# Performance work log

Measured on AMD Instinct MI355X. Metric: run time of the kernel, lower is better.

## Reference

```python
import jax, jax.numpy as jnp
import numpy as np

V, BLOCK, D, H, L = 32000, 2048, 768, 12, 4
B, T = 2, 2048
HD = D // H
FF = 4 * D


def setup_inputs() -> dict:
    key = jax.random.key(0)
    ks = jax.random.split(key, 20)
    s = 0.02
    inp = {
        "idx": jax.random.randint(ks[0], (B, T), 0, V),
        "tok_emb": jax.random.normal(ks[1], (V, D), jnp.float32) * s,
        "pos_emb": jax.random.normal(ks[2], (BLOCK, D), jnp.float32) * s,
        # per-layer stacked params (leading dim L); linear weights stored [in, out]
        "ln1_w": jnp.ones((L, D), jnp.float32),
        "ln1_b": jnp.zeros((L, D), jnp.float32),
        "Wqkv": jax.random.normal(ks[3], (L, D, 3 * D), jnp.float32) * s,
        "bqkv": jnp.zeros((L, 3 * D), jnp.float32),
        "Wproj": jax.random.normal(ks[4], (L, D, D), jnp.float32) * s,
        "bproj": jnp.zeros((L, D), jnp.float32),
        "ln2_w": jnp.ones((L, D), jnp.float32),
        "ln2_b": jnp.zeros((L, D), jnp.float32),
        "Wfc": jax.random.normal(ks[5], (L, D, FF), jnp.float32) * s,
        "bfc": jnp.zeros((L, FF), jnp.float32),
        "Wfc2": jax.random.normal(ks[6], (L, FF, D), jnp.float32) * s,
        "bfc2": jnp.zeros((L, D), jnp.float32),
        "lnf_w": jnp.ones((D,), jnp.float32),
        "lnf_b": jnp.zeros((D,), jnp.float32),
    }
    return inp


def _layernorm(x, w, b, eps=1e-5):
    mu = jnp.mean(x, axis=-1, keepdims=True)
    var = jnp.var(x, axis=-1, keepdims=True)
    return (x - mu) * jax.lax.rsqrt(var + eps) * w + b


def _attn(x, Wqkv, bqkv, Wproj, bproj):
    b, t, c = x.shape
    qkv = x @ Wqkv + bqkv  # [B,T,3D]
    q, k, v = jnp.split(qkv, 3, axis=-1)
    q = q.reshape(b, t, H, HD)
    k = k.reshape(b, t, H, HD)
    v = v.reshape(b, t, H, HD)
    scale = 1.0 / np.sqrt(HD)
    att = jnp.einsum("bthd,bshd->bhts", q, k) * scale  # [B,H,T,T]
    causal = jnp.tril(jnp.ones((t, t), bool))
    att = jnp.where(causal[None, None], att, -jnp.inf)
    att = jax.nn.softmax(att, axis=-1)
    out = jnp.einsum("bhts,bshd->bthd", att, v).reshape(b, t, c)
    return out @ Wproj + bproj


def reference(idx, tok_emb, pos_emb, ln1_w, ln1_b, Wqkv, bqkv, Wproj, bproj,
              ln2_w, ln2_b, Wfc, bfc, Wfc2, bfc2, lnf_w, lnf_b):
    t = idx.shape[1]
    x = tok_emb[idx] + pos_emb[:t][None]  # [B,T,D]
    for l in range(L):
        h = _layernorm(x, ln1_w[l], ln1_b[l])
        x = x + _attn(h, Wqkv[l], bqkv[l], Wproj[l], bproj[l])
        h = _layernorm(x, ln2_w[l], ln2_b[l])
        h = jax.nn.gelu(h @ Wfc[l] + bfc[l], approximate=False) @ Wfc2[l] + bfc2[l]
        x = x + h
    x = _layernorm(x, lnf_w, lnf_b)
    return x @ tok_emb.T  # tied head, [B,T,V]
```

## Files before the change

kernel.cpp:

```cpp
#include <hip/hip_runtime.h>
#include <math.h>

#define VOCAB  32000
#define DMODEL 768
#define NHEAD  12
#define NLAYER 4
#define BATCH  2
#define SEQ    2048
#define HEADD  64
#define FFDIM  3072
#define MROWS  (BATCH*SEQ)

typedef __attribute__((ext_vector_type(8))) short bf16x8;
typedef __attribute__((ext_vector_type(4))) float f32x4;

__device__ __forceinline__ unsigned short f2bf(float f) {
    union { float f; unsigned u; } v; v.f = f;
    unsigned r = v.u + 0x7fffu + ((v.u >> 16) & 1u);
    return (unsigned short)(r >> 16);
}

__device__ __forceinline__ bf16x8 pack8(const float* v) {
    union { unsigned short u[8]; bf16x8 v8; } un;
#pragma unroll
    for (int j = 0; j < 8; j++) un.u[j] = f2bf(v[j]);
    return un.v8;
}

__global__ void cvt_bf16_x4(const float* __restrict__ in, unsigned short* __restrict__ out, int n4) {
    int i = blockIdx.x * blockDim.x + threadIdx.x;
    if (i >= n4) return;
    float4 v = ((const float4*)in)[i];
    uint2 o;
    o.x = (unsigned)f2bf(v.x) | ((unsigned)f2bf(v.y) << 16);
    o.y = (unsigned)f2bf(v.z) | ((unsigned)f2bf(v.w) << 16);
    ((uint2*)out)[i] = o;
}

__global__ void transpose_cvt(const float* __restrict__ W, unsigned short* __restrict__ Wt,
                              int Kdim, int Ndim) {
    __shared__ float tile[32][33];
    int l  = blockIdx.z;
    int k0 = blockIdx.x * 32;
    int n0 = blockIdx.y * 32;
    const float* Wl = W + (size_t)l * Kdim * Ndim;
    unsigned short* Wtl = Wt + (size_t)l * Kdim * Ndim;
    int c = threadIdx.x & 31, r = threadIdx.x >> 5;
#pragma unroll
    for (int i = 0; i < 4; i++)
        tile[r + i * 8][c] = Wl[(size_t)(k0 + r + i * 8) * Ndim + n0 + c];
    __syncthreads();
#pragma unroll
    for (int i = 0; i < 4; i++)
        Wtl[(size_t)(n0 + r + i * 8) * Kdim + k0 + c] = f2bf(tile[c][r + i * 8]);
}

__global__ void embed_kernel(const int* __restrict__ idx, const float* __restrict__ tok,
                             const float* __restrict__ pos, float* __restrict__ x) {
    int row = blockIdx.x;
    int t = row & (SEQ - 1);
    int tr = idx[row];
    const float4* ts = (const float4*)(tok + (size_t)tr * DMODEL);
    const float4* ps = (const float4*)(pos + (size_t)t * DMODEL);
    float4* xs = (float4*)(x + (size_t)row * DMODEL);
    int i = threadIdx.x;
    float4 a = ts[i], b = ps[i];
    xs[i] = make_float4(a.x + b.x, a.y + b.y, a.z + b.z, a.w + b.w);
}

__global__ void layernorm_kernel(const float* __restrict__ x, const float* __restrict__ w,
                                 const float* __restrict__ b, unsigned short* __restrict__ out) {
    int row = blockIdx.x;
    const float* xr = x + (size_t)row * DMODEL;
    int t = threadIdx.x;
    float v0 = xr[t], v1 = xr[t + 256], v2 = xr[t + 512];
    float s = v0 + v1 + v2;
    float ss = v0 * v0 + v1 * v1 + v2 * v2;
#pragma unroll
    for (int off = 32; off >= 1; off >>= 1) {
        s  += __shfl_xor(s, off);
        ss += __shfl_xor(ss, off);
    }
    __shared__ float red[8];
    int wave = t >> 6, lane = t & 63;
    if (lane == 0) { red[wave] = s; red[wave + 4] = ss; }
    __syncthreads();
    s  = red[0] + red[1] + red[2] + red[3];
    ss = red[4] + red[5] + red[6] + red[7];
    float mu = s * (1.0f / DMODEL);
    float var = ss * (1.0f / DMODEL) - mu * mu;
    float rs = rsqrtf(var + 1e-5f);
    unsigned short* orow = out + (size_t)row * DMODEL;
    orow[t]       = f2bf((v0 - mu) * rs * w[t]       + b[t]);
    orow[t + 256] = f2bf((v1 - mu) * rs * w[t + 256] + b[t + 256]);
    orow[t + 512] = f2bf((v2 - mu) * rs * w[t + 512] + b[t + 512]);
}

template <bool GELU_, bool RESID_, bool OUTBF16_, bool BIAS_>
__global__ __launch_bounds__(256) void gemm_kernel(
    const unsigned short* __restrict__ A,
    const unsigned short* __restrict__ Bw,
    const float* __restrict__ bias,
    const float* resid,
    float* Cf, unsigned short* Cb,
    int Ndim, int Kdim) {
    const int bm = blockIdx.x * 128;
    const int bn = blockIdx.y * 128;
    __shared__ unsigned short As[128][40];
    __shared__ unsigned short Bs[128][40];
    int tid = threadIdx.x;
    int wave = tid >> 6, lane = tid & 63;
    int wm = (wave >> 1) * 64, wn = (wave & 1) * 64;
    int quad = lane >> 4, ln = lane & 15;
    f32x4 acc[4][4] = {};

    for (int k0 = 0; k0 < Kdim; k0 += 32) {
        __syncthreads();
#pragma unroll
        for (int i = 0; i < 2; i++) {
            int c = tid + i * 256;
            int r = c >> 2, col = (c & 3) * 8;
            bf16x8 av = *(const bf16x8*)(A  + (size_t)(bm + r) * Kdim + k0 + col);
            *(bf16x8*)(&As[r][col]) = av;
            bf16x8 bv = *(const bf16x8*)(Bw + (size_t)(bn + r) * Kdim + k0 + col);
            *(bf16x8*)(&Bs[r][col]) = bv;
        }
        __syncthreads();
        bf16x8 af[4], bfr[4];
#pragma unroll
        for (int tm = 0; tm < 4; tm++) af[tm]  = *(const bf16x8*)(&As[wm + tm * 16 + ln][quad * 8]);
#pragma unroll
        for (int tn = 0; tn < 4; tn++) bfr[tn] = *(const bf16x8*)(&Bs[wn + tn * 16 + ln][quad * 8]);
#pragma unroll
        for (int tm = 0; tm < 4; tm++)
#pragma unroll
            for (int tn = 0; tn < 4; tn++)
                acc[tm][tn] = __builtin_amdgcn_mfma_f32_16x16x32_bf16(af[tm], bfr[tn], acc[tm][tn], 0, 0, 0);
    }

#pragma unroll
    for (int tm = 0; tm < 4; tm++)
#pragma unroll
        for (int tn = 0; tn < 4; tn++)
#pragma unroll
            for (int r = 0; r < 4; r++) {
                int row = bm + wm + tm * 16 + quad * 4 + r;
                int col = bn + wn + tn * 16 + ln;
                float c = acc[tm][tn][r];
                if (BIAS_) c += bias[col];
                if (GELU_) c = 0.5f * c * (1.0f + erff(c * 0.70710678118654752f));
                if (RESID_) c += resid[(size_t)row * Ndim + col];
                if (OUTBF16_) Cb[(size_t)row * Ndim + col] = f2bf(c);
                else          Cf[(size_t)row * Ndim + col] = c;
            }
}

__global__ __launch_bounds__(256) void attn_kernel(const float* __restrict__ qkv,
                                                   unsigned short* __restrict__ out) {
    int qtile = blockIdx.x;
    int bh = blockIdx.y;
    int b = bh / NHEAD, h = bh % NHEAD;
    int q0 = qtile * 128;
    const float* base = qkv + (size_t)b * SEQ * (3 * DMODEL);

    __shared__ unsigned short Qs[128][72];
    __shared__ unsigned short Ks[64][72];
    __shared__ unsigned short Vs[64][72];
    __shared__ unsigned short Ps[128][72];

    int tid = threadIdx.x, wave = tid >> 6, lane = tid & 63;
    int quad = lane >> 4, ln = lane & 15;

    for (int c = tid; c < 1024; c += 256) {
        int r = c >> 3, col = (c & 7) * 8;
        const float* src = base + (size_t)(q0 + r) * (3 * DMODEL) + h * HEADD + col;
        float4 a = *(const float4*)src, bb = *(const float4*)(src + 4);
        float tmp[8] = {a.x, a.y, a.z, a.w, bb.x, bb.y, bb.z, bb.w};
        *(bf16x8*)(&Qs[r][col]) = pack8(tmp);
    }
    __syncthreads();

    bf16x8 qf[2][2];
#pragma unroll
    for (int tm = 0; tm < 2; tm++)
#pragma unroll
        for (int ks = 0; ks < 2; ks++)
            qf[tm][ks] = *(const bf16x8*)(&Qs[wave * 32 + tm * 16 + ln][ks * 32 + quad * 8]);

    f32x4 o[2][4] = {};
    float mst[8], lst[8];
#pragma unroll
    for (int i = 0; i < 8; i++) { mst[i] = -3.0e38f; lst[i] = 0.0f; }

    const float scale = 0.125f;
    int nkt = qtile * 2 + 2;

    for (int kt = 0; kt < nkt; kt++) {
        __syncthreads();
        for (int c = tid; c < 512; c += 256) {
            int r = c >> 3, col = (c & 7) * 8;
            const float* sk = base + (size_t)(kt * 64 + r) * (3 * DMODEL) + DMODEL + h * HEADD + col;
            float4 a = *(const float4*)sk, bb = *(const float4*)(sk + 4);
            float tmp[8] = {a.x, a.y, a.z, a.w, bb.x, bb.y, bb.z, bb.w};
            *(bf16x8*)(&Ks[r][col]) = pack8(tmp);
            const float* sv = base + (size_t)(kt * 64 + r) * (3 * DMODEL) + 2 * DMODEL + h * HEADD + col;
            float4 va = *(const float4*)sv, vb = *(const float4*)(sv + 4);
            float tv[8] = {va.x, va.y, va.z, va.w, vb.x, vb.y, vb.z, vb.w};
#pragma unroll
            for (int j = 0; j < 8; j++) Vs[col + j][r] = f2bf(tv[j]);
        }
        __syncthreads();

        f32x4 s[2][4];
#pragma unroll
        for (int tm = 0; tm < 2; tm++)
#pragma unroll
            for (int tn = 0; tn < 4; tn++) s[tm][tn] = (f32x4){0.f, 0.f, 0.f, 0.f};
        bf16x8 kf[4][2];
#pragma unroll
        for (int tn = 0; tn < 4; tn++)
#pragma unroll
            for (int ks = 0; ks < 2; ks++)
                kf[tn][ks] = *(const bf16x8*)(&Ks[tn * 16 + ln][ks * 32 + quad * 8]);
#pragma unroll
        for (int tm = 0; tm < 2; tm++)
#pragma unroll
            for (int tn = 0; tn < 4; tn++)
#pragma unroll
                for (int ks = 0; ks < 2; ks++)
                    s[tm][tn] = __builtin_amdgcn_mfma_f32_16x16x32_bf16(qf[tm][ks], kf[tn][ks], s[tm][tn], 0, 0, 0);

#pragma unroll
        for (int tm = 0; tm < 2; tm++)
#pragma unroll
            for (int tn = 0; tn < 4; tn++)
#pragma unroll
                for (int r = 0; r < 4; r++) {
                    int qi = q0 + wave * 32 + tm * 16 + quad * 4 + r;
                    int kj = kt * 64 + tn * 16 + ln;
                    float sv = s[tm][tn][r] * scale;
                    s[tm][tn][r] = (kj > qi) ? -3.0e38f : sv;
                }

#pragma unroll
        for (int tm = 0; tm < 2; tm++)
#pragma unroll
            for (int r = 0; r < 4; r++) {
                float mx = fmaxf(fmaxf(s[tm][0][r], s[tm][1][r]), fmaxf(s[tm][2][r], s[tm][3][r]));
#pragma unroll
                for (int msk = 1; msk <= 8; msk <<= 1) mx = fmaxf(mx, __shfl_xor(mx, msk));
                int ri = tm * 4 + r;
                float mnew = fmaxf(mst[ri], mx);
                float alpha = __expf(mst[ri] - mnew);
                mst[ri] = mnew;
                float psum = 0.f;
#pragma unroll
                for (int tn = 0; tn < 4; tn++) {
                    float p = __expf(s[tm][tn][r] - mnew);
                    s[tm][tn][r] = p;
                    psum += p;
                }
#pragma unroll
                for (int msk = 1; msk <= 8; msk <<= 1) psum += __shfl_xor(psum, msk);
                lst[ri] = lst[ri] * alpha + psum;
#pragma unroll
                for (int nd = 0; nd < 4; nd++) o[tm][nd][r] *= alpha;
            }

#pragma unroll
        for (int tm = 0; tm < 2; tm++)
#pragma unroll
            for (int tn = 0; tn < 4; tn++)
#pragma unroll
                for (int r = 0; r < 4; r++)
                    Ps[wave * 32 + tm * 16 + quad * 4 + r][tn * 16 + ln] = f2bf(s[tm][tn][r]);

        bf16x8 pf[2][2], vf[4][2];
#pragma unroll
        for (int tm = 0; tm < 2; tm++)
#pragma unroll
            for (int ks = 0; ks < 2; ks++)
                pf[tm][ks] = *(const bf16x8*)(&Ps[wave * 32 + tm * 16 + ln][ks * 32 + quad * 8]);
#pragma unroll
        for (int nd = 0; nd < 4; nd++)
#pragma unroll
            for (int ks = 0; ks < 2; ks++)
                vf[nd][ks] = *(const bf16x8*)(&Vs[nd * 16 + ln][ks * 32 + quad * 8]);
#pragma unroll
        for (int tm = 0; tm < 2; tm++)
#pragma unroll
            for (int nd = 0; nd < 4; nd++)
#pragma unroll
                for (int ks = 0; ks < 2; ks++)
                    o[tm][nd] = __builtin_amdgcn_mfma_f32_16x16x32_bf16(pf[tm][ks], vf[nd][ks], o[tm][nd], 0, 0, 0);
    }

#pragma unroll
    for (int tm = 0; tm < 2; tm++)
#pragma unroll
        for (int r = 0; r < 4; r++) {
            float inv = 1.0f / lst[tm * 4 + r];
            int trow = q0 + wave * 32 + tm * 16 + quad * 4 + r;
#pragma unroll
            for (int nd = 0; nd < 4; nd++) {
                int col = h * HEADD + nd * 16 + ln;
                out[(size_t)(b * SEQ + trow) * DMODEL + col] = f2bf(o[tm][nd][r] * inv);
            }
        }
}

extern "C" void kernel_launch(void* const* d_in, const int* in_sizes, int n_in,
                              void* d_out, int out_size, void* d_ws, size_t ws_size,
                              hipStream_t stream) {
    const int*   idx   = (const int*)  d_in[0];
    const float* tok   = (const float*)d_in[1];
    const float* pos   = (const float*)d_in[2];
    const float* ln1w  = (const float*)d_in[3];
    const float* ln1b  = (const float*)d_in[4];
    const float* Wqkv  = (const float*)d_in[5];
    const float* bqkv  = (const float*)d_in[6];
    const float* Wproj = (const float*)d_in[7];
    const float* bproj = (const float*)d_in[8];
    const float* ln2w  = (const float*)d_in[9];
    const float* ln2b  = (const float*)d_in[10];
    const float* Wfc   = (const float*)d_in[11];
    const float* bfc   = (const float*)d_in[12];
    const float* Wfc2  = (const float*)d_in[13];
    const float* bfc2  = (const float*)d_in[14];
    const float* lnfw  = (const float*)d_in[15];
    const float* lnfb  = (const float*)d_in[16];

    char* ob = (char*)d_out;
    float*          qkv    = (float*)(ob + 0);
    float*          x      = (float*)(ob + 37748736);
    unsigned short* ffact  = (unsigned short*)(ob + 50331648);
    unsigned short* attnb  = (unsigned short*)(ob + 75497472);
    unsigned short* WqkvT  = (unsigned short*)(ob + 81788928);
    unsigned short* WprojT = (unsigned short*)(ob + 95944704);
    unsigned short* WfcT   = (unsigned short*)(ob + 100663296);
    unsigned short* Wfc2T  = (unsigned short*)(ob + 119537664);
    unsigned short* tokT   = (unsigned short*)d_ws;
    unsigned short* lnout  = (unsigned short*)((char*)d_ws + 49152000);

    cvt_bf16_x4<<<24000, 256, 0, stream>>>(tok, tokT, VOCAB * DMODEL / 4);
    transpose_cvt<<<dim3(24, 72, NLAYER), 256, 0, stream>>>(Wqkv,  WqkvT,  DMODEL, 3 * DMODEL);
    transpose_cvt<<<dim3(24, 24, NLAYER), 256, 0, stream>>>(Wproj, WprojT, DMODEL, DMODEL);
    transpose_cvt<<<dim3(24, 96, NLAYER), 256, 0, stream>>>(Wfc,   WfcT,   DMODEL, FFDIM);
    transpose_cvt<<<dim3(96, 24, NLAYER), 256, 0, stream>>>(Wfc2,  Wfc2T,  FFDIM,  DMODEL);

    embed_kernel<<<MROWS, 192, 0, stream>>>(idx, tok, pos, x);

    for (int l = 0; l < NLAYER; l++) {
        layernorm_kernel<<<MROWS, 256, 0, stream>>>(x, ln1w + l * DMODEL, ln1b + l * DMODEL, lnout);
        gemm_kernel<false, false, false, true><<<dim3(32, 18), 256, 0, stream>>>(
            lnout, WqkvT + (size_t)l * 3 * DMODEL * DMODEL, bqkv + l * 3 * DMODEL,
            nullptr, qkv, nullptr, 3 * DMODEL, DMODEL);
        attn_kernel<<<dim3(16, BATCH * NHEAD), 256, 0, stream>>>(qkv, attnb);
        gemm_kernel<false, true, false, true><<<dim3(32, 6), 256, 0, stream>>>(
            attnb, WprojT + (size_t)l * DMODEL * DMODEL, bproj + l * DMODEL,
            x, x, nullptr, DMODEL, DMODEL);
        layernorm_kernel<<<MROWS, 256, 0, stream>>>(x, ln2w + l * DMODEL, ln2b + l * DMODEL, lnout);
        gemm_kernel<true, false, true, true><<<dim3(32, 24), 256, 0, stream>>>(
            lnout, WfcT + (size_t)l * FFDIM * DMODEL, bfc + l * FFDIM,
            nullptr, nullptr, ffact, FFDIM, DMODEL);
        gemm_kernel<false, true, false, true><<<dim3(32, 6), 256, 0, stream>>>(
            ffact, Wfc2T + (size_t)l * FFDIM * DMODEL, bfc2 + l * DMODEL,
            x, x, nullptr, DMODEL, FFDIM);
    }

    layernorm_kernel<<<MROWS, 256, 0, stream>>>(x, lnfw, lnfb, lnout);
    gemm_kernel<false, false, false, false><<<dim3(32, 250), 256, 0, stream>>>(
        lnout, tokT, nullptr, nullptr, (float*)d_out, nullptr, VOCAB, DMODEL);
}
```

Before: 2.332 ms.

## Use async global-to-LDS loads in GEMM and store QKV as bf16

The GEMM tile loads now use global_load_lds to copy 16-byte chunks straight into unpadded LDS tiles, skipping the round trip through registers. The QKV projection now writes bf16 instead of fp32, so the attention kernel reads half the bytes and no longer converts per tile. The output buffer offsets are repacked to match. Removing the LDS padding may cause bank conflicts on fragment reads, and bf16 QKV adds rounding before attention, though attention already converted to bf16.

```diff
diff --git a/kernel.cpp b/kernel.cpp
--- a/kernel.cpp
+++ b/kernel.cpp
@@ -20,11 +20,10 @@
     return (unsigned short)(r >> 16);
 }
 
-__device__ __forceinline__ bf16x8 pack8(const float* v) {
-    union { unsigned short u[8]; bf16x8 v8; } un;
-#pragma unroll
-    for (int j = 0; j < 8; j++) un.u[j] = f2bf(v[j]);
-    return un.v8;
+__device__ __forceinline__ void async_lds16(const unsigned short* g, unsigned short* l) {
+    __builtin_amdgcn_global_load_lds(
+        (const __attribute__((address_space(1))) unsigned int*)(const void*)g,
+        (__attribute__((address_space(3))) unsigned int*)(void*)l, 16, 0, 0);
 }
 
 __global__ void cvt_bf16_x4(const float* __restrict__ in, unsigned short* __restrict__ out, int n4) {
@@ -106,24 +105,23 @@
     int Ndim, int Kdim) {
     const int bm = blockIdx.x * 128;
     const int bn = blockIdx.y * 128;
-    __shared__ unsigned short As[128][40];
-    __shared__ unsigned short Bs[128][40];
+    __shared__ unsigned short As[128][32];
+    __shared__ unsigned short Bs[128][32];
     int tid = threadIdx.x;
     int wave = tid >> 6, lane = tid & 63;
     int wm = (wave >> 1) * 64, wn = (wave & 1) * 64;
     int quad = lane >> 4, ln = lane & 15;
+    int srow = lane >> 2;
+    int scol = (lane & 3) * 8;
     f32x4 acc[4][4] = {};
 
     for (int k0 = 0; k0 < Kdim; k0 += 32) {
         __syncthreads();
 #pragma unroll
         for (int i = 0; i < 2; i++) {
-            int c = tid + i * 256;
-            int r = c >> 2, col = (c & 3) * 8;
-            bf16x8 av = *(const bf16x8*)(A  + (size_t)(bm + r) * Kdim + k0 + col);
-            *(bf16x8*)(&As[r][col]) = av;
-            bf16x8 bv = *(const bf16x8*)(Bw + (size_t)(bn + r) * Kdim + k0 + col);
-            *(bf16x8*)(&Bs[r][col]) = bv;
+            int ch = (wave << 1) | i;
+            async_lds16(A  + (size_t)(bm + ch * 16 + srow) * Kdim + k0 + scol, &As[ch * 16][0]);
+            async_lds16(Bw + (size_t)(bn + ch * 16 + srow) * Kdim + k0 + scol, &Bs[ch * 16][0]);
         }
         __syncthreads();
         bf16x8 af[4], bfr[4];
@@ -155,13 +153,13 @@
             }
 }
 
-__global__ __launch_bounds__(256) void attn_kernel(const float* __restrict__ qkv,
+__global__ __launch_bounds__(256) void attn_kernel(const unsigned short* __restrict__ qkv,
                                                    unsigned short* __restrict__ out) {
     int qtile = blockIdx.x;
     int bh = blockIdx.y;
     int b = bh / NHEAD, h = bh % NHEAD;
     int q0 = qtile * 128;
-    const float* base = qkv + (size_t)b * SEQ * (3 * DMODEL);
+    const unsigned short* base = qkv + (size_t)b * SEQ * (3 * DMODEL);
 
     __shared__ unsigned short Qs[128][72];
     __shared__ unsigned short Ks[64][72];
@@ -173,10 +171,8 @@
 
     for (int c = tid; c < 1024; c += 256) {
         int r = c >> 3, col = (c & 7) * 8;
-        const float* src = base + (size_t)(q0 + r) * (3 * DMODEL) + h * HEADD + col;
-        float4 a = *(const float4*)src, bb = *(const float4*)(src + 4);
-        float tmp[8] = {a.x, a.y, a.z, a.w, bb.x, bb.y, bb.z, bb.w};
-        *(bf16x8*)(&Qs[r][col]) = pack8(tmp);
+        *(bf16x8*)(&Qs[r][col]) =
+            *(const bf16x8*)(base + (size_t)(q0 + r) * (3 * DMODEL) + h * HEADD + col);
     }
     __syncthreads();
 
@@ -199,15 +195,12 @@
         __syncthreads();
         for (int c = tid; c < 512; c += 256) {
             int r = c >> 3, col = (c & 7) * 8;
-            const float* sk = base + (size_t)(kt * 64 + r) * (3 * DMODEL) + DMODEL + h * HEADD + col;
-            float4 a = *(const float4*)sk, bb = *(const float4*)(sk + 4);
-            float tmp[8] = {a.x, a.y, a.z, a.w, bb.x, bb.y, bb.z, bb.w};
-            *(bf16x8*)(&Ks[r][col]) = pack8(tmp);
-            const float* sv = base + (size_t)(kt * 64 + r) * (3 * DMODEL) + 2 * DMODEL + h * HEADD + col;
-            float4 va = *(const float4*)sv, vb = *(const float4*)(sv + 4);
-            float tv[8] = {va.x, va.y, va.z, va.w, vb.x, vb.y, vb.z, vb.w};
-#pragma unroll
-            for (int j = 0; j < 8; j++) Vs[col + j][r] = f2bf(tv[j]);
+            *(bf16x8*)(&Ks[r][col]) =
+                *(const bf16x8*)(base + (size_t)(kt * 64 + r) * (3 * DMODEL) + DMODEL + h * HEADD + col);
+            union { bf16x8 v; unsigned short u[8]; } vv;
+            vv.v = *(const bf16x8*)(base + (size_t)(kt * 64 + r) * (3 * DMODEL) + 2 * DMODEL + h * HEADD + col);
+#pragma unroll
+            for (int j = 0; j < 8; j++) Vs[col + j][r] = vv.u[j];
         }
         __syncthreads();
 
@@ -331,14 +324,14 @@
     const float* lnfb  = (const float*)d_in[16];
 
     char* ob = (char*)d_out;
-    float*          qkv    = (float*)(ob + 0);
-    float*          x      = (float*)(ob + 37748736);
-    unsigned short* ffact  = (unsigned short*)(ob + 50331648);
-    unsigned short* attnb  = (unsigned short*)(ob + 75497472);
-    unsigned short* WqkvT  = (unsigned short*)(ob + 81788928);
-    unsigned short* WprojT = (unsigned short*)(ob + 95944704);
-    unsigned short* WfcT   = (unsigned short*)(ob + 100663296);
-    unsigned short* Wfc2T  = (unsigned short*)(ob + 119537664);
+    unsigned short* qkvb   = (unsigned short*)(ob + 0);
+    float*          x      = (float*)(ob + 18874368);
+    unsigned short* ffact  = (unsigned short*)(ob + 31457280);
+    unsigned short* attnb  = (unsigned short*)(ob + 56623104);
+    unsigned short* WqkvT  = (unsigned short*)(ob + 62914560);
+    unsigned short* WprojT = (unsigned short*)(ob + 77070336);
+    unsigned short* WfcT   = (unsigned short*)(ob + 81788928);
+    unsigned short* Wfc2T  = (unsigned short*)(ob + 100663296);
     unsigned short* tokT   = (unsigned short*)d_ws;
     unsigned short* lnout  = (unsigned short*)((char*)d_ws + 49152000);
 
@@ -352,10 +345,10 @@
 
     for (int l = 0; l < NLAYER; l++) {
         layernorm_kernel<<<MROWS, 256, 0, stream>>>(x, ln1w + l * DMODEL, ln1b + l * DMODEL, lnout);
-        gemm_kernel<false, false, false, true><<<dim3(32, 18), 256, 0, stream>>>(
+        gemm_kernel<false, false, true, true><<<dim3(32, 18), 256, 0, stream>>>(
             lnout, WqkvT + (size_t)l * 3 * DMODEL * DMODEL, bqkv + l * 3 * DMODEL,
-            nullptr, qkv, nullptr, 3 * DMODEL, DMODEL);
-        attn_kernel<<<dim3(16, BATCH * NHEAD), 256, 0, stream>>>(qkv, attnb);
+            nullptr, nullptr, qkvb, 3 * DMODEL, DMODEL);
+        attn_kernel<<<dim3(16, BATCH * NHEAD), 256, 0, stream>>>(qkvb, attnb);
         gemm_kernel<false, true, false, true><<<dim3(32, 6), 256, 0, stream>>>(
             attnb, WprojT + (size_t)l * DMODEL * DMODEL, bproj + l * DMODEL,
             x, x, nullptr, DMODEL, DMODEL);
```

Result: faster. 2.267 ms (-2.8%).
